# Performance work log

Hardware: AMD Instinct MI355X
Metric: run time of the kernel (lower is better)

## Reference

```python
import jax, jax.numpy as jnp
import numpy as np

N = 262144        # tokens routed
D = 1024          # input_dim
E = 64            # num_experts
TOP_K = 2
NOISE_EPS = 1e-05
ALPHA = 10.0


def setup_inputs() -> dict:
    key = jax.random.key(0)
    k1, k2, k3, k4, k5 = jax.random.split(key, 5)
    x = jax.random.normal(k1, (N, D), dtype=jnp.float32)
    # nn.Linear init scale ~ 1/sqrt(fan_in); keep logits at sane magnitude
    gate_w = jax.random.normal(k2, (E, D), dtype=jnp.float32) * (1.0 / np.sqrt(D))
    gate_b = jax.random.normal(k3, (E,), dtype=jnp.float32) * 0.01
    # w_noise is initialized to zeros in the module; use small random values
    # so the noise path is exercised
    w_noise = jax.random.normal(k4, (E, E), dtype=jnp.float32) * 0.01
    noise = jax.random.normal(k5, (N, E), dtype=jnp.float32)  # torch.randn_like
    return {"x": x, "gate_w": gate_w, "gate_b": gate_b,
            "w_noise": w_noise, "noise": noise}


def reference(x, gate_w, gate_b, w_noise, noise):
    # gate linear: [N, D] @ [D, E] + [E]
    clean_logits = jnp.einsum('nd,ed->ne', x, gate_w) + gate_b
    # training-mode learnable noise injection
    raw_noise_stddev = clean_logits @ w_noise                 # [N, E]
    noise_stddev = jax.nn.softplus(raw_noise_stddev) + NOISE_EPS
    logits = clean_logits + noise * noise_stddev              # noisy_logits

    # decompostion_tp: k-th largest per row (kthvalue(n - k + 1) == k-th largest)
    kth_largest = jax.lax.top_k(logits, TOP_K)[0][:, -1]       # [N]
    mask = logits < kth_largest[:, None]                       # strictly below kth
    sm = jax.nn.softmax(logits, axis=1)
    out = jnp.where(mask,
                    ALPHA * jnp.log1p(sm),      # alpha * log(sm + 1)
                    ALPHA * jnp.expm1(sm))      # alpha * (exp(sm) - 1)

    gates = jax.nn.softmax(out, axis=1)
    return gates
```

## Files before the change

kernel.cpp:

```cpp
#include <hip/hip_runtime.h>

typedef _Float16 half8v __attribute__((ext_vector_type(8)));
typedef _Float16 half4v __attribute__((ext_vector_type(4)));
typedef float f32x4 __attribute__((ext_vector_type(4)));

constexpr float INV4096 = 1.0f / 4096.0f;
constexpr float ALPHA = 10.0f;

__device__ __forceinline__ f32x4 mfma16(half8v a, half8v b, f32x4 c_) {
  return __builtin_amdgcn_mfma_f32_16x16x32_f16(a, b, c_, 0, 0, 0);
}

__global__ __launch_bounds__(256, 2) void topk_gating(
    const float *__restrict__ X, const float *__restrict__ GW,
    const float *__restrict__ GB, const float *__restrict__ WN,
    const float *__restrict__ NZ, float *__restrict__ OUT) {
  __shared__ __align__(16) char lds[49152];
  const int tid = threadIdx.x;
  const int lane = tid & 63;
  const int wv = tid >> 6;
  const int q = lane >> 4;
  const int c = lane & 15;
  const int waveRow = blockIdx.x * 64 + wv * 16;

  const int bE0 = tid >> 4;
  const int bCC = tid & 15;

#pragma unroll
  for (int i = 0; i < 4; ++i) {
    int idx4 = tid + i * 256;
    int k = idx4 >> 4;
    int e0 = (idx4 & 15) << 2;
    f32x4 v = *reinterpret_cast<const f32x4 *>(WN + k * 64 + e0);
#pragma unroll
    for (int j = 0; j < 4; ++j) {
      int e = e0 + j;
      float vv = v[j];
      _Float16 hh = (_Float16)vv;
      _Float16 ll = (_Float16)((vv - (float)hh) * 4096.0f);
      int off = e * 128 + ((((k >> 3) ^ (e & 7))) << 4) + ((k & 7) << 1);
      *reinterpret_cast<_Float16 *>(lds + 32768 + off) = hh;
      *reinterpret_cast<_Float16 *>(lds + 40960 + off) = ll;
    }
  }

  f32x4 accH[4] = {};
  f32x4 accX[4] = {};
  f32x4 aCur[4], aNxt[4], bCur[4], bNxt[4];

  const float *xBase = X + (size_t)(waveRow + c) * 1024 + q * 8;
  aCur[0] = *(const f32x4 *)(xBase + 0);
  aCur[1] = *(const f32x4 *)(xBase + 4);
  aCur[2] = *(const f32x4 *)(xBase + 32);
  aCur[3] = *(const f32x4 *)(xBase + 36);
#pragma unroll
  for (int i = 0; i < 4; ++i)
    bCur[i] = *(const f32x4 *)(GW + (size_t)(bE0 + 16 * i) * 1024 + bCC * 4);
#pragma unroll
  for (int i = 0; i < 4; ++i) {
    int e = bE0 + 16 * i;
    half4v h, l;
#pragma unroll
    for (int j = 0; j < 4; ++j) {
      float vv = bCur[i][j];
      _Float16 hh = (_Float16)vv;
      h[j] = hh;
      l[j] = (_Float16)((vv - (float)hh) * 4096.0f);
    }
    int off = e * 128 + ((((bCC >> 1) ^ (e & 7))) << 4) + ((bCC & 1) << 3);
    *reinterpret_cast<half4v *>(lds + off) = h;
    *reinterpret_cast<half4v *>(lds + 8192 + off) = l;
  }
  __syncthreads();

  for (int kc = 0; kc < 16; ++kc) {
    if (kc < 15) {
      const float *xb = xBase + (kc + 1) * 64;
      aNxt[0] = *(const f32x4 *)(xb + 0);
      aNxt[1] = *(const f32x4 *)(xb + 4);
      aNxt[2] = *(const f32x4 *)(xb + 32);
      aNxt[3] = *(const f32x4 *)(xb + 36);
#pragma unroll
      for (int i = 0; i < 4; ++i)
        bNxt[i] = *(const f32x4 *)(GW + (size_t)(bE0 + 16 * i) * 1024 +
                                   (kc + 1) * 64 + bCC * 4);
    }
    const int buf = (kc & 1) * 16384;
#pragma unroll
    for (int ks = 0; ks < 2; ++ks) {
      half8v ah, al;
#pragma unroll
      for (int j = 0; j < 8; ++j) {
        float xv = aCur[ks * 2 + (j >> 2)][j & 3];
        _Float16 hh = (_Float16)xv;
        ah[j] = hh;
        al[j] = (_Float16)((xv - (float)hh) * 4096.0f);
      }
#pragma unroll
      for (int t = 0; t < 4; ++t) {
        int e = t * 16 + c;
        int off = buf + e * 128 + ((((ks * 4 + q) ^ (e & 7))) << 4);
        half8v bh = *reinterpret_cast<half8v *>(lds + off);
        half8v bl = *reinterpret_cast<half8v *>(lds + 8192 + off);
        accH[t] = mfma16(ah, bh, accH[t]);
        accX[t] = mfma16(ah, bl, accX[t]);
        accX[t] = mfma16(al, bh, accX[t]);
      }
    }
    if (kc < 15) {
      const int wbuf = ((kc + 1) & 1) * 16384;
#pragma unroll
      for (int i = 0; i < 4; ++i) {
        int e = bE0 + 16 * i;
        half4v h, l;
#pragma unroll
        for (int j = 0; j < 4; ++j) {
          float vv = bNxt[i][j];
          _Float16 hh = (_Float16)vv;
          h[j] = hh;
          l[j] = (_Float16)((vv - (float)hh) * 4096.0f);
        }
        int off = wbuf + e * 128 + ((((bCC >> 1) ^ (e & 7))) << 4) + ((bCC & 1) << 3);
        *reinterpret_cast<half4v *>(lds + off) = h;
        *reinterpret_cast<half4v *>(lds + 8192 + off) = l;
      }
#pragma unroll
      for (int i = 0; i < 4; ++i) aCur[i] = aNxt[i];
    }
    __syncthreads();
  }

  float cl[4][4];
#pragma unroll
  for (int t = 0; t < 4; ++t) {
    float bs = GB[t * 16 + c];
#pragma unroll
    for (int r = 0; r < 4; ++r)
      cl[t][r] = accH[t][r] + accX[t][r] * INV4096 + bs;
  }

  float nz[4][4];
#pragma unroll
  for (int t = 0; t < 4; ++t)
#pragma unroll
    for (int r = 0; r < 4; ++r)
      nz[t][r] = NZ[(size_t)(waveRow + 4 * q + r) * 64 + t * 16 + c];

  char *cb = lds + wv * 4096;
#pragma unroll
  for (int t = 0; t < 4; ++t)
#pragma unroll
    for (int r = 0; r < 4; ++r) {
      int row = 4 * q + r;
      int colf = t * 16 + c;
      int off = row * 256 + ((((colf >> 2) ^ row)) << 4) + ((colf & 3) << 2);
      *reinterpret_cast<float *>(cb + off) = cl[t][r];
    }
  __syncthreads();

  f32x4 rH[4] = {};
  f32x4 rX[4] = {};
#pragma unroll
  for (int ks = 0; ks < 2; ++ks) {
    int slot0 = ks * 8 + q * 2;
    f32x4 a0 = *reinterpret_cast<f32x4 *>(cb + c * 256 + (((slot0 ^ c)) << 4));
    f32x4 a1 = *reinterpret_cast<f32x4 *>(cb + c * 256 + ((((slot0 + 1) ^ c)) << 4));
    half8v ah, al;
#pragma unroll
    for (int j = 0; j < 4; ++j) {
      float v = a0[j];
      _Float16 hh = (_Float16)v;
      ah[j] = hh;
      al[j] = (_Float16)((v - (float)hh) * 4096.0f);
      float v2 = a1[j];
      _Float16 h2 = (_Float16)v2;
      ah[4 + j] = h2;
      al[4 + j] = (_Float16)((v2 - (float)h2) * 4096.0f);
    }
#pragma unroll
    for (int t = 0; t < 4; ++t) {
      int e = t * 16 + c;
      int off = 32768 + e * 128 + ((((ks * 4 + q) ^ (e & 7))) << 4);
      half8v bh = *reinterpret_cast<half8v *>(lds + off);
      half8v bl = *reinterpret_cast<half8v *>(lds + 8192 + off);
      rH[t] = mfma16(ah, bh, rH[t]);
      rX[t] = mfma16(ah, bl, rX[t]);
      rX[t] = mfma16(al, bh, rX[t]);
    }
  }

  float logits[4][4];
#pragma unroll
  for (int t = 0; t < 4; ++t)
#pragma unroll
    for (int r = 0; r < 4; ++r) {
      float raw = rH[t][r] + rX[t][r] * INV4096;
      float sp = fmaxf(raw, 0.0f) + __logf(1.0f + __expf(-fabsf(raw)));
      logits[t][r] = cl[t][r] + nz[t][r] * (sp + 1e-5f);
    }

  float m1v[4], m2v[4];
#pragma unroll
  for (int r = 0; r < 4; ++r) {
    float v0 = logits[0][r], v1 = logits[1][r], v2 = logits[2][r], v3 = logits[3][r];
    float a = fmaxf(v0, v1), b = fminf(v0, v1);
    float d1 = fmaxf(v2, v3), d2 = fminf(v2, v3);
    float m1 = fmaxf(a, d1);
    float m2 = fmaxf(fminf(a, d1), fmaxf(b, d2));
#pragma unroll
    for (int s = 1; s <= 8; s <<= 1) {
      float om1 = __shfl_xor(m1, s, 64);
      float om2 = __shfl_xor(m2, s, 64);
      float hi = fmaxf(m1, om1);
      float lo = fminf(m1, om1);
      float sec = (m1 >= om1) ? m2 : om2;
      m2 = fmaxf(lo, sec);
      m1 = hi;
    }
    m1v[r] = m1;
    m2v[r] = m2;
  }

  float sme[4][4];
  float ssum[4] = {0.f, 0.f, 0.f, 0.f};
#pragma unroll
  for (int t = 0; t < 4; ++t)
#pragma unroll
    for (int r = 0; r < 4; ++r) {
      float e_ = __expf(logits[t][r] - m1v[r]);
      sme[t][r] = e_;
      ssum[r] += e_;
    }
#pragma unroll
  for (int r = 0; r < 4; ++r) {
#pragma unroll
    for (int s = 1; s <= 8; s <<= 1) ssum[r] += __shfl_xor(ssum[r], s, 64);
  }

  float outv[4][4];
#pragma unroll
  for (int r = 0; r < 4; ++r) {
    float inv = 1.0f / ssum[r];
#pragma unroll
    for (int t = 0; t < 4; ++t) {
      float sm = sme[t][r] * inv;
      float vlog = ALPHA * __logf(1.0f + sm);
      float vexp = ALPHA * (__expf(sm) - 1.0f);
      outv[t][r] = (logits[t][r] < m2v[r]) ? vlog : vexp;
    }
  }

  float gmax[4];
#pragma unroll
  for (int r = 0; r < 4; ++r) {
    float g = fmaxf(fmaxf(outv[0][r], outv[1][r]), fmaxf(outv[2][r], outv[3][r]));
#pragma unroll
    for (int s = 1; s <= 8; s <<= 1) g = fmaxf(g, __shfl_xor(g, s, 64));
    gmax[r] = g;
  }
  float gsum[4] = {0.f, 0.f, 0.f, 0.f};
#pragma unroll
  for (int t = 0; t < 4; ++t)
#pragma unroll
    for (int r = 0; r < 4; ++r) {
      float e_ = __expf(outv[t][r] - gmax[r]);
      outv[t][r] = e_;
      gsum[r] += e_;
    }
#pragma unroll
  for (int r = 0; r < 4; ++r) {
#pragma unroll
    for (int s = 1; s <= 8; s <<= 1) gsum[r] += __shfl_xor(gsum[r], s, 64);
  }
#pragma unroll
  for (int r = 0; r < 4; ++r) {
    float ginv = 1.0f / gsum[r];
    size_t rowOff = (size_t)(waveRow + 4 * q + r) * 64;
#pragma unroll
    for (int t = 0; t < 4; ++t)
      OUT[rowOff + t * 16 + c] = outv[t][r] * ginv;
  }
}

extern "C" void kernel_launch(void *const *d_in, const int *in_sizes, int n_in,
                              void *d_out, int out_size, void *d_ws,
                              size_t ws_size, hipStream_t stream) {
  const float *x = (const float *)d_in[0];
  const float *gw = (const float *)d_in[1];
  const float *gb = (const float *)d_in[2];
  const float *wn = (const float *)d_in[3];
  const float *nz = (const float *)d_in[4];
  float *out = (float *)d_out;
  const int N = in_sizes[0] / 1024;
  dim3 grid(N / 64), block(256);
  hipLaunchKernelGGL(topk_gating, grid, block, 0, stream, x, gw, gb, wn, nz, out);
}
```

Baseline: 285.3 us.

## Presplit gate weights into workspace and DMA them directly into LDS

A small pre-kernel converts gate_w and w_noise into the swizzled fp16 hi/lo layout once per call and writes it to workspace. The main kernel then streams those tiles into LDS with global_load_lds, dropping the per-block fp32 loads and split/convert VALU work. Less LDS is used, so occupancy can rise to 3 blocks per CU. The softmax epilogue is also restructured per row to lower register pressure. The cost is an extra kernel launch and a workspace round trip.

```diff
diff --git a/kernel.cpp b/kernel.cpp
--- a/kernel.cpp
+++ b/kernel.cpp
@@ -1,7 +1,6 @@
 #include <hip/hip_runtime.h>
 
 typedef _Float16 half8v __attribute__((ext_vector_type(8)));
-typedef _Float16 half4v __attribute__((ext_vector_type(4)));
 typedef float f32x4 __attribute__((ext_vector_type(4)));
 
 constexpr float INV4096 = 1.0f / 4096.0f;
@@ -11,11 +10,56 @@
   return __builtin_amdgcn_mfma_f32_16x16x32_f16(a, b, c_, 0, 0, 0);
 }
 
-__global__ __launch_bounds__(256, 2) void topk_gating(
-    const float *__restrict__ X, const float *__restrict__ GW,
-    const float *__restrict__ GB, const float *__restrict__ WN,
-    const float *__restrict__ NZ, float *__restrict__ OUT) {
-  __shared__ __align__(16) char lds[49152];
+__device__ __forceinline__ void dma16(const void *g, void *l) {
+  __builtin_amdgcn_global_load_lds(
+      (const __attribute__((address_space(1))) void *)g,
+      (__attribute__((address_space(3))) void *)l, 16, 0, 0);
+}
+
+__global__ __launch_bounds__(256) void presplit(const float *__restrict__ GW,
+                                                const float *__restrict__ WN,
+                                                char *__restrict__ ws) {
+  const int b = blockIdx.x;
+  const int tid = threadIdx.x;
+  if (b < 64) {
+    int idx = b * 256 + tid;
+    int e = idx >> 8;
+    int c4 = idx & 255;
+    f32x4 v = *reinterpret_cast<const f32x4 *>(GW + (size_t)idx * 4);
+#pragma unroll
+    for (int j = 0; j < 4; ++j) {
+      int k = c4 * 4 + j;
+      float vv = v[j];
+      _Float16 hh = (_Float16)vv;
+      _Float16 ll = (_Float16)((vv - (float)hh) * 4096.0f);
+      int ck = k >> 6, kk = k & 63;
+      int off = ck * 16384 + e * 128 + ((((kk >> 3) ^ (e & 7))) << 4) + ((kk & 7) << 1);
+      *reinterpret_cast<_Float16 *>(ws + off) = hh;
+      *reinterpret_cast<_Float16 *>(ws + off + 8192) = ll;
+    }
+  } else {
+    int idx = (b - 64) * 256 + tid;
+    int k = idx >> 4;
+    int e0 = (idx & 15) << 2;
+    f32x4 v = *reinterpret_cast<const f32x4 *>(WN + (size_t)k * 64 + e0);
+#pragma unroll
+    for (int j = 0; j < 4; ++j) {
+      int e = e0 + j;
+      float vv = v[j];
+      _Float16 hh = (_Float16)vv;
+      _Float16 ll = (_Float16)((vv - (float)hh) * 4096.0f);
+      int off = 262144 + e * 128 + ((((k >> 3) ^ (e & 7))) << 4) + ((k & 7) << 1);
+      *reinterpret_cast<_Float16 *>(ws + off) = hh;
+      *reinterpret_cast<_Float16 *>(ws + off + 8192) = ll;
+    }
+  }
+}
+
+__global__ __launch_bounds__(256, 3) void topk_gating(
+    const float *__restrict__ X, const char *__restrict__ WS,
+    const float *__restrict__ GB, const float *__restrict__ NZ,
+    float *__restrict__ OUT) {
+  __shared__ __align__(16) char lds[32768];
   const int tid = threadIdx.x;
   const int lane = tid & 63;
   const int wv = tid >> 6;
@@ -23,30 +67,9 @@
   const int c = lane & 15;
   const int waveRow = blockIdx.x * 64 + wv * 16;
 
-  const int bE0 = tid >> 4;
-  const int bCC = tid & 15;
-
-#pragma unroll
-  for (int i = 0; i < 4; ++i) {
-    int idx4 = tid + i * 256;
-    int k = idx4 >> 4;
-    int e0 = (idx4 & 15) << 2;
-    f32x4 v = *reinterpret_cast<const f32x4 *>(WN + k * 64 + e0);
-#pragma unroll
-    for (int j = 0; j < 4; ++j) {
-      int e = e0 + j;
-      float vv = v[j];
-      _Float16 hh = (_Float16)vv;
-      _Float16 ll = (_Float16)((vv - (float)hh) * 4096.0f);
-      int off = e * 128 + ((((k >> 3) ^ (e & 7))) << 4) + ((k & 7) << 1);
-      *reinterpret_cast<_Float16 *>(lds + 32768 + off) = hh;
-      *reinterpret_cast<_Float16 *>(lds + 40960 + off) = ll;
-    }
-  }
-
   f32x4 accH[4] = {};
   f32x4 accX[4] = {};
-  f32x4 aCur[4], aNxt[4], bCur[4], bNxt[4];
+  f32x4 aCur[4], aNxt[4];
 
   const float *xBase = X + (size_t)(waveRow + c) * 1024 + q * 8;
   aCur[0] = *(const f32x4 *)(xBase + 0);
@@ -55,22 +78,7 @@
   aCur[3] = *(const f32x4 *)(xBase + 36);
 #pragma unroll
   for (int i = 0; i < 4; ++i)
-    bCur[i] = *(const f32x4 *)(GW + (size_t)(bE0 + 16 * i) * 1024 + bCC * 4);
-#pragma unroll
-  for (int i = 0; i < 4; ++i) {
-    int e = bE0 + 16 * i;
-    half4v h, l;
-#pragma unroll
-    for (int j = 0; j < 4; ++j) {
-      float vv = bCur[i][j];
-      _Float16 hh = (_Float16)vv;
-      h[j] = hh;
-      l[j] = (_Float16)((vv - (float)hh) * 4096.0f);
-    }
-    int off = e * 128 + ((((bCC >> 1) ^ (e & 7))) << 4) + ((bCC & 1) << 3);
-    *reinterpret_cast<half4v *>(lds + off) = h;
-    *reinterpret_cast<half4v *>(lds + 8192 + off) = l;
-  }
+    dma16(WS + i * 4096 + wv * 1024 + lane * 16, lds + i * 4096 + wv * 1024);
   __syncthreads();
 
   for (int kc = 0; kc < 16; ++kc) {
@@ -80,10 +88,12 @@
       aNxt[1] = *(const f32x4 *)(xb + 4);
       aNxt[2] = *(const f32x4 *)(xb + 32);
       aNxt[3] = *(const f32x4 *)(xb + 36);
+      const int wbuf = ((kc + 1) & 1) * 16384;
+      const char *src = WS + (kc + 1) * 16384;
 #pragma unroll
       for (int i = 0; i < 4; ++i)
-        bNxt[i] = *(const f32x4 *)(GW + (size_t)(bE0 + 16 * i) * 1024 +
-                                   (kc + 1) * 64 + bCC * 4);
+        dma16(src + i * 4096 + wv * 1024 + lane * 16,
+              lds + wbuf + i * 4096 + wv * 1024);
     }
     const int buf = (kc & 1) * 16384;
 #pragma unroll
@@ -101,34 +111,30 @@
         int e = t * 16 + c;
         int off = buf + e * 128 + ((((ks * 4 + q) ^ (e & 7))) << 4);
         half8v bh = *reinterpret_cast<half8v *>(lds + off);
-        half8v bl = *reinterpret_cast<half8v *>(lds + 8192 + off);
+        half8v bl = *reinterpret_cast<half8v *>(lds + off + 8192);
         accH[t] = mfma16(ah, bh, accH[t]);
         accX[t] = mfma16(ah, bl, accX[t]);
         accX[t] = mfma16(al, bh, accX[t]);
       }
     }
     if (kc < 15) {
-      const int wbuf = ((kc + 1) & 1) * 16384;
-#pragma unroll
-      for (int i = 0; i < 4; ++i) {
-        int e = bE0 + 16 * i;
-        half4v h, l;
-#pragma unroll
-        for (int j = 0; j < 4; ++j) {
-          float vv = bNxt[i][j];
-          _Float16 hh = (_Float16)vv;
-          h[j] = hh;
-          l[j] = (_Float16)((vv - (float)hh) * 4096.0f);
-        }
-        int off = wbuf + e * 128 + ((((bCC >> 1) ^ (e & 7))) << 4) + ((bCC & 1) << 3);
-        *reinterpret_cast<half4v *>(lds + off) = h;
-        *reinterpret_cast<half4v *>(lds + 8192 + off) = l;
-      }
 #pragma unroll
       for (int i = 0; i < 4; ++i) aCur[i] = aNxt[i];
     }
     __syncthreads();
   }
+
+  float nz[4][4];
+#pragma unroll
+  for (int t = 0; t < 4; ++t)
+#pragma unroll
+    for (int r = 0; r < 4; ++r)
+      nz[t][r] = NZ[(size_t)(waveRow + 4 * q + r) * 64 + t * 16 + c];
+
+#pragma unroll
+  for (int i = 0; i < 4; ++i)
+    dma16(WS + 262144 + i * 4096 + wv * 1024 + lane * 16,
+          lds + i * 4096 + wv * 1024);
 
   float cl[4][4];
 #pragma unroll
@@ -139,14 +145,7 @@
       cl[t][r] = accH[t][r] + accX[t][r] * INV4096 + bs;
   }
 
-  float nz[4][4];
-#pragma unroll
-  for (int t = 0; t < 4; ++t)
-#pragma unroll
-    for (int r = 0; r < 4; ++r)
-      nz[t][r] = NZ[(size_t)(waveRow + 4 * q + r) * 64 + t * 16 + c];
-
-  char *cb = lds + wv * 4096;
+  char *cb = lds + 16384 + wv * 4096;
 #pragma unroll
   for (int t = 0; t < 4; ++t)
 #pragma unroll
@@ -180,33 +179,32 @@
 #pragma unroll
     for (int t = 0; t < 4; ++t) {
       int e = t * 16 + c;
-      int off = 32768 + e * 128 + ((((ks * 4 + q) ^ (e & 7))) << 4);
+      int off = e * 128 + ((((ks * 4 + q) ^ (e & 7))) << 4);
       half8v bh = *reinterpret_cast<half8v *>(lds + off);
-      half8v bl = *reinterpret_cast<half8v *>(lds + 8192 + off);
+      half8v bl = *reinterpret_cast<half8v *>(lds + off + 8192);
       rH[t] = mfma16(ah, bh, rH[t]);
       rX[t] = mfma16(ah, bl, rX[t]);
       rX[t] = mfma16(al, bh, rX[t]);
     }
   }
 
-  float logits[4][4];
+  float lg[4][4];
 #pragma unroll
   for (int t = 0; t < 4; ++t)
 #pragma unroll
     for (int r = 0; r < 4; ++r) {
       float raw = rH[t][r] + rX[t][r] * INV4096;
       float sp = fmaxf(raw, 0.0f) + __logf(1.0f + __expf(-fabsf(raw)));
-      logits[t][r] = cl[t][r] + nz[t][r] * (sp + 1e-5f);
-    }
-
-  float m1v[4], m2v[4];
+      lg[r][t] = cl[t][r] + nz[t][r] * (sp + 1e-5f);
+    }
+
 #pragma unroll
   for (int r = 0; r < 4; ++r) {
-    float v0 = logits[0][r], v1 = logits[1][r], v2 = logits[2][r], v3 = logits[3][r];
-    float a = fmaxf(v0, v1), b = fminf(v0, v1);
+    float v0 = lg[r][0], v1 = lg[r][1], v2 = lg[r][2], v3 = lg[r][3];
+    float a = fmaxf(v0, v1), b_ = fminf(v0, v1);
     float d1 = fmaxf(v2, v3), d2 = fminf(v2, v3);
     float m1 = fmaxf(a, d1);
-    float m2 = fmaxf(fminf(a, d1), fmaxf(b, d2));
+    float m2 = fmaxf(fminf(a, d1), fmaxf(b_, d2));
 #pragma unroll
     for (int s = 1; s <= 8; s <<= 1) {
       float om1 = __shfl_xor(m1, s, 64);
@@ -217,68 +215,39 @@
       m2 = fmaxf(lo, sec);
       m1 = hi;
     }
-    m1v[r] = m1;
-    m2v[r] = m2;
-  }
-
-  float sme[4][4];
-  float ssum[4] = {0.f, 0.f, 0.f, 0.f};
-#pragma unroll
-  for (int t = 0; t < 4; ++t)
-#pragma unroll
-    for (int r = 0; r < 4; ++r) {
-      float e_ = __expf(logits[t][r] - m1v[r]);
-      sme[t][r] = e_;
-      ssum[r] += e_;
-    }
-#pragma unroll
-  for (int r = 0; r < 4; ++r) {
-#pragma unroll
-    for (int s = 1; s <= 8; s <<= 1) ssum[r] += __shfl_xor(ssum[r], s, 64);
-  }
-
-  float outv[4][4];
-#pragma unroll
-  for (int r = 0; r < 4; ++r) {
-    float inv = 1.0f / ssum[r];
-#pragma unroll
-    for (int t = 0; t < 4; ++t) {
-      float sm = sme[t][r] * inv;
+    float se[4], ssum = 0.f;
+#pragma unroll
+    for (int t = 0; t < 4; ++t) {
+      se[t] = __expf(lg[r][t] - m1);
+      ssum += se[t];
+    }
+#pragma unroll
+    for (int s = 1; s <= 8; s <<= 1) ssum += __shfl_xor(ssum, s, 64);
+    float inv = 1.0f / ssum;
+    float ov[4];
+#pragma unroll
+    for (int t = 0; t < 4; ++t) {
+      float sm = se[t] * inv;
       float vlog = ALPHA * __logf(1.0f + sm);
       float vexp = ALPHA * (__expf(sm) - 1.0f);
-      outv[t][r] = (logits[t][r] < m2v[r]) ? vlog : vexp;
-    }
-  }
-
-  float gmax[4];
-#pragma unroll
-  for (int r = 0; r < 4; ++r) {
-    float g = fmaxf(fmaxf(outv[0][r], outv[1][r]), fmaxf(outv[2][r], outv[3][r]));
+      ov[t] = (lg[r][t] < m2) ? vlog : vexp;
+    }
+    float g = fmaxf(fmaxf(ov[0], ov[1]), fmaxf(ov[2], ov[3]));
 #pragma unroll
     for (int s = 1; s <= 8; s <<= 1) g = fmaxf(g, __shfl_xor(g, s, 64));
-    gmax[r] = g;
-  }
-  float gsum[4] = {0.f, 0.f, 0.f, 0.f};
-#pragma unroll
-  for (int t = 0; t < 4; ++t)
-#pragma unroll
-    for (int r = 0; r < 4; ++r) {
-      float e_ = __expf(outv[t][r] - gmax[r]);
-      outv[t][r] = e_;
-      gsum[r] += e_;
-    }
-#pragma unroll
-  for (int r = 0; r < 4; ++r) {
-#pragma unroll
-    for (int s = 1; s <= 8; s <<= 1) gsum[r] += __shfl_xor(gsum[r], s, 64);
-  }
-#pragma unroll
-  for (int r = 0; r < 4; ++r) {
-    float ginv = 1.0f / gsum[r];
+    float gsum = 0.f;
+#pragma unroll
+    for (int t = 0; t < 4; ++t) {
+      ov[t] = __expf(ov[t] - g);
+      gsum += ov[t];
+    }
+#pragma unroll
+    for (int s = 1; s <= 8; s <<= 1) gsum += __shfl_xor(gsum, s, 64);
+    float ginv = 1.0f / gsum;
     size_t rowOff = (size_t)(waveRow + 4 * q + r) * 64;
 #pragma unroll
     for (int t = 0; t < 4; ++t)
-      OUT[rowOff + t * 16 + c] = outv[t][r] * ginv;
+      OUT[rowOff + t * 16 + c] = ov[t] * ginv;
   }
 }
 
@@ -291,7 +260,10 @@
   const float *wn = (const float *)d_in[3];
   const float *nz = (const float *)d_in[4];
   float *out = (float *)d_out;
+  char *ws = (char *)d_ws;
   const int N = in_sizes[0] / 1024;
-  dim3 grid(N / 64), block(256);
-  hipLaunchKernelGGL(topk_gating, grid, block, 0, stream, x, gw, gb, wn, nz, out);
-}
+
+  hipLaunchKernelGGL(presplit, dim3(68), dim3(256), 0, stream, gw, wn, ws);
+  hipLaunchKernelGGL(topk_gating, dim3(N / 64), dim3(256), 0, stream, x, ws,
+                     gb, nz, out);
+}
```

After: 283.3 us. About the same (-0.7%).
